# Kernel tuning notes

Hardware: AMD Instinct MI355X
Metric: run time of the kernel (lower is better)

Reference implementation:

```python
import jax, jax.numpy as jnp
import numpy as np

B, H, S, D = 2, 16, 2048, 64

def setup_inputs() -> dict:
    key = jax.random.key(0)
    kq, kk, kv, km = jax.random.split(key, 4)
    Query = jax.random.normal(kq, (B, H, S, D), dtype=jnp.float32)
    Key = jax.random.normal(kk, (B, H, S, D), dtype=jnp.float32)
    Value = jax.random.normal(kv, (B, H, S, D), dtype=jnp.float32)
    attention_mask = jax.random.randint(km, (B, 1, S, S), 0, 2).astype(jnp.bool_)
    return {"Query": Query, "Key": Key, "Value": Value,
            "attention_mask": attention_mask, "dim_key": D}

def reference(Query, Key, Value, attention_mask, dim_key):
    # scores: [B,H,S,S]
    scale = 1.0 / np.sqrt(dim_key).astype(np.float32)
    scores = jnp.einsum('bhqd,bhkd->bhqk', Query, Key) * scale
    scores = jnp.where(attention_mask, jnp.float32(-1e9), scores)
    attention = jax.nn.softmax(scores, axis=-1)
    context = jnp.einsum('bhqk,bhkd->bhqd', attention, Value)
    return (context, attention)
```

## Files before the change

kernel.cpp:

```cpp
#include <hip/hip_runtime.h>
#include <hip/hip_bf16.h>


#define S_LEN 2048
#define D_DIM 64
#define LOG2E 1.44269504088896340736f

typedef __attribute__((ext_vector_type(8))) short bf16x8;
typedef __attribute__((ext_vector_type(4))) float f32x4;
typedef unsigned long long u64;

#define FENCE() asm volatile("" ::: "memory")

__device__ __forceinline__ unsigned int f2bs2(float x, float y) {
    union { __hip_bfloat162 h; unsigned int u; } u;
    u.h = __float22bfloat162_rn(make_float2(x, y));
    return u.u;
}
__device__ __forceinline__ short f2bs(float f) {
    union { __hip_bfloat16 h; short s; } u;
    u.h = __float2bfloat16(f);
    return u.s;
}
__device__ __forceinline__ bf16x8 cvt8(float4 a, float4 b) {
    union { bf16x8 v; unsigned int w[4]; } u;
    u.w[0] = f2bs2(a.x, a.y); u.w[1] = f2bs2(a.z, a.w);
    u.w[2] = f2bs2(b.x, b.y); u.w[3] = f2bs2(b.z, b.w);
    return u.v;
}

__device__ __forceinline__ void gl2lds16(const short* g, short* l) {
    __builtin_amdgcn_global_load_lds(
        (const __attribute__((address_space(1))) unsigned int*)g,
        (__attribute__((address_space(3))) unsigned int*)l, 16, 0, 0);
}

__global__ __launch_bounds__(256) void prep_kv(const float* __restrict__ K,
                                               const float* __restrict__ V,
                                               short* __restrict__ Kb,
                                               short* __restrict__ Vtb) {
    __shared__ short T[64 * 80];
    const int bh = blockIdx.x >> 5;
    const int kt = blockIdx.x & 31;
    const int k0 = kt * 64;
    const int t  = threadIdx.x;
    const int row = t >> 2;
    const int cq  = (t & 3) * 16;

    const size_t base = (size_t)bh * S_LEN * D_DIM;
    {
        const float* kp = K + base + (size_t)(k0 + row) * D_DIM + cq;
        float4 a = ((const float4*)kp)[0], b = ((const float4*)kp)[1],
               c = ((const float4*)kp)[2], d = ((const float4*)kp)[3];
        short* op = Kb + base + (size_t)(k0 + row) * D_DIM + cq;
        *(bf16x8*)op       = cvt8(a, b);
        *(bf16x8*)(op + 8) = cvt8(c, d);
    }
    {
        const float* vp = V + base + (size_t)(k0 + row) * D_DIM + cq;
        float4 a = ((const float4*)vp)[0], b = ((const float4*)vp)[1],
               c = ((const float4*)vp)[2], d = ((const float4*)vp)[3];
        float vv[16] = {a.x,a.y,a.z,a.w, b.x,b.y,b.z,b.w,
                        c.x,c.y,c.z,c.w, d.x,d.y,d.z,d.w};
        #pragma unroll
        for (int i = 0; i < 16; ++i)
            T[(cq + i) * 80 + row] = f2bs(vv[i]);
    }
    __syncthreads();
    {
        const int d  = t >> 2;
        const int kc = (t & 3) * 16;
        short* op = Vtb + (size_t)bh * D_DIM * S_LEN + (size_t)d * S_LEN + k0 + kc;
        *(bf16x8*)op       = *(const bf16x8*)&T[d * 80 + kc];
        *(bf16x8*)(op + 8) = *(const bf16x8*)&T[d * 80 + kc + 8];
    }
}

__global__ __launch_bounds__(256) void mask_pack(const int* __restrict__ M,
                                                 u64* __restrict__ Mp) {
    const int lane = threadIdx.x & 63;
    const int wid  = (blockIdx.x * 256 + threadIdx.x) >> 6;
    const int nwaves = gridDim.x * 4;
    const int nwords = 2 * S_LEN * (S_LEN / 64);
    for (int w = wid; w < nwords; w += nwaves) {
        int v = M[(size_t)w * 64 + lane];
        u64 bits = __ballot(v != 0);
        if (lane == 0) Mp[w] = bits;
    }
}

__global__ __launch_bounds__(256, 4) void sdpa_main(
    const float* __restrict__ Q, const short* __restrict__ Kb,
    const short* __restrict__ Vtb, const u64* __restrict__ Mp,
    float* __restrict__ Ctx, float* __restrict__ Attn)
{
    __shared__ short Kt[2][64 * 64];
    __shared__ short Pt[4 * 16 * 80];

    const int tid  = threadIdx.x;
    const int wave = tid >> 6;
    const int lane = tid & 63;
    const int quad = lane >> 4;
    const int l16  = lane & 15;

    const int bid = blockIdx.x;
    const int bh  = ((bid >> 8) << 3) | (bid & 7);
    const int qt  = (bid >> 3) & 31;
    const int b   = bh >> 4;
    const int qw  = qt * 64 + wave * 16;

    const size_t sd_off = (size_t)bh * S_LEN * D_DIM;
    const float* Qbh = Q + sd_off;
    const short* Kbh = Kb + sd_off;
    const short* Vbh = Vtb + (size_t)bh * D_DIM * S_LEN;
    float* Cbh = Ctx + sd_off;
    float* Abh = Attn + (size_t)bh * S_LEN * S_LEN;

    const short* vfp = Vbh + (size_t)l16 * S_LEN + quad * 8;

    bf16x8 qfrag[2];
    {
        const int qrow = qw + l16;
        const float s = 0.125f * LOG2E;
        #pragma unroll
        for (int kc = 0; kc < 2; ++kc) {
            const float* qp = Qbh + (size_t)qrow * D_DIM + kc * 32 + quad * 8;
            float4 a = ((const float4*)qp)[0], c = ((const float4*)qp)[1];
            a.x*=s; a.y*=s; a.z*=s; a.w*=s; c.x*=s; c.y*=s; c.z*=s; c.w*=s;
            qfrag[kc] = cvt8(a, c);
        }
    }

    const u64* mp = Mp + (size_t)(b * S_LEN + qw + quad * 4) * (S_LEN / 64);

    u64 mw[4], mwn[4];
    float lacc[4] = {0.f, 0.f, 0.f, 0.f};

    #pragma unroll
    for (int r = 0; r < 4; ++r) mw[r] = mp[r * 32];
    #pragma unroll
    for (int rd = 0; rd < 2; ++rd) {
        const int m = tid + rd * 256;
        const int row = m >> 3, sc = m & 7, c = sc ^ (row & 7);
        gl2lds16(Kbh + (size_t)row * D_DIM + c * 8, &Kt[0][m * 8]);
    }
    FENCE();

#define S1_STEP(KT) do {                                                        \
    const int kt_ = (KT);                                                       \
    const int tn_ = (kt_ + 1) & 31; const int p_ = kt_ & 1;                     \
    _Pragma("unroll") for (int r = 0; r < 4; ++r) mwn[r] = mp[r * 32 + tn_];    \
    FENCE();                                                                    \
    asm volatile("s_waitcnt vmcnt(4)" ::: "memory");                            \
    __builtin_amdgcn_s_barrier();                                               \
    __builtin_amdgcn_sched_barrier(0);                                          \
    _Pragma("unroll") for (int rd = 0; rd < 2; ++rd) {                          \
        const int m_ = tid + rd * 256;                                          \
        const int row_ = m_ >> 3, sc_ = m_ & 7, c_ = sc_ ^ (row_ & 7);          \
        gl2lds16(Kbh + (size_t)(tn_ * 64 + row_) * D_DIM + c_ * 8,              \
                 &Kt[p_ ^ 1][m_ * 8]);                                          \
    }                                                                           \
    FENCE();                                                                    \
    __builtin_amdgcn_s_setprio(1);                                              \
    _Pragma("unroll") for (int cc = 0; cc < 4; ++cc) {                          \
        const int keyl_ = cc * 16 + l16;                                        \
        f32x4 acc_ = {0.f, 0.f, 0.f, 0.f};                                      \
        bf16x8 b0_ = *(const bf16x8*)&Kt[p_][keyl_ * 64 + ((quad) ^ (keyl_ & 7)) * 8];      \
        bf16x8 b1_ = *(const bf16x8*)&Kt[p_][keyl_ * 64 + ((4 + quad) ^ (keyl_ & 7)) * 8];  \
        acc_ = __builtin_amdgcn_mfma_f32_16x16x32_bf16(qfrag[0], b0_, acc_, 0, 0, 0);       \
        acc_ = __builtin_amdgcn_mfma_f32_16x16x32_bf16(qfrag[1], b1_, acc_, 0, 0, 0);       \
        _Pragma("unroll") for (int r = 0; r < 4; ++r) {                         \
            float pe_ = __builtin_amdgcn_exp2f(acc_[r]);                        \
            pe_ = ((mw[r] >> keyl_) & 1ull) ? 0.f : pe_;                        \
            lacc[r] += pe_;                                                     \
        }                                                                       \
    }                                                                           \
    __builtin_amdgcn_s_setprio(0);                                              \
    _Pragma("unroll") for (int r = 0; r < 4; ++r) mw[r] = mwn[r];               \
} while (0)

    #pragma unroll 1
    for (int kt = 0; kt < 32; ++kt) S1_STEP(kt);

    #pragma unroll
    for (int off = 1; off < 16; off <<= 1) {
        #pragma unroll
        for (int r = 0; r < 4; ++r) lacc[r] += __shfl_xor(lacc[r], off, 64);
    }
    float inv_l[4];
    #pragma unroll
    for (int r = 0; r < 4; ++r) inv_l[r] = 1.0f / lacc[r];

    f32x4 cacc[4];
    #pragma unroll
    for (int dc = 0; dc < 4; ++dc) cacc[dc] = (f32x4){0.f, 0.f, 0.f, 0.f};
    short* Pw = &Pt[wave * 16 * 80];

#define S2_STEP(KT, WSTR) do {                                                  \
    const int kt_ = (KT); const int k0_ = kt_ * 64;                             \
    const int tn_ = (kt_ + 1) & 31; const int p_ = kt_ & 1;                     \
    _Pragma("unroll") for (int r = 0; r < 4; ++r) mwn[r] = mp[r * 32 + tn_];    \
    bf16x8 vfr[2][4];                                                           \
    _Pragma("unroll") for (int kc = 0; kc < 2; ++kc)                            \
        _Pragma("unroll") for (int dc = 0; dc < 4; ++dc)                        \
            vfr[kc][dc] = *(const bf16x8*)(vfp + (size_t)dc * 16 * S_LEN + k0_ + kc * 32);  \
    FENCE();                                                                    \
    asm volatile("s_waitcnt vmcnt(" WSTR ")" ::: "memory");                     \
    __builtin_amdgcn_s_barrier();                                               \
    __builtin_amdgcn_sched_barrier(0);                                          \
    _Pragma("unroll") for (int rd = 0; rd < 2; ++rd) {                          \
        const int m_ = tid + rd * 256;                                          \
        const int row_ = m_ >> 3, sc_ = m_ & 7, c_ = sc_ ^ (row_ & 7);          \
        gl2lds16(Kbh + (size_t)(tn_ * 64 + row_) * D_DIM + c_ * 8,              \
                 &Kt[p_ ^ 1][m_ * 8]);                                          \
    }                                                                           \
    FENCE();                                                                    \
    __builtin_amdgcn_s_setprio(1);                                              \
    float* ap0_ = Abh + (size_t)(qw + quad * 4) * S_LEN + k0_;                  \
    _Pragma("unroll") for (int cc = 0; cc < 4; ++cc) {                          \
        const int keyl_ = cc * 16 + l16;                                        \
        f32x4 acc_ = {0.f, 0.f, 0.f, 0.f};                                      \
        bf16x8 b0_ = *(const bf16x8*)&Kt[p_][keyl_ * 64 + ((quad) ^ (keyl_ & 7)) * 8];      \
        bf16x8 b1_ = *(const bf16x8*)&Kt[p_][keyl_ * 64 + ((4 + quad) ^ (keyl_ & 7)) * 8];  \
        acc_ = __builtin_amdgcn_mfma_f32_16x16x32_bf16(qfrag[0], b0_, acc_, 0, 0, 0);       \
        acc_ = __builtin_amdgcn_mfma_f32_16x16x32_bf16(qfrag[1], b1_, acc_, 0, 0, 0);       \
        _Pragma("unroll") for (int r = 0; r < 4; ++r) {                         \
            float pe_ = __builtin_amdgcn_exp2f(acc_[r]);                        \
            pe_ = ((mw[r] >> keyl_) & 1ull) ? 0.f : pe_;                        \
            __builtin_nontemporal_store(pe_ * inv_l[r], ap0_ + (size_t)r * S_LEN + keyl_);  \
            Pw[(quad * 4 + r) * 80 + keyl_] = f2bs(pe_);    \
        }                                                                       \
    }                                                                           \
    __builtin_amdgcn_s_setprio(0);                                              \
    FENCE();                                                                    \
    _Pragma("unroll") for (int kc = 0; kc < 2; ++kc) {                          \
        bf16x8 af_ = *(const bf16x8*)&Pw[l16 * 80 + kc * 32 + quad * 8];        \
        _Pragma("unroll") for (int dc = 0; dc < 4; ++dc)                        \
            cacc[dc] = __builtin_amdgcn_mfma_f32_16x16x32_bf16(af_, vfr[kc][dc], cacc[dc], 0, 0, 0); \
    }                                                                           \
    _Pragma("unroll") for (int r = 0; r < 4; ++r) mw[r] = mwn[r];               \
} while (0)

    S2_STEP(0, "12");
    #pragma unroll 1
    for (int kt = 1; kt < 32; ++kt) S2_STEP(kt, "28");

    #pragma unroll
    for (int dc = 0; dc < 4; ++dc) {
        #pragma unroll
        for (int r = 0; r < 4; ++r) {
            Cbh[(size_t)(qw + quad * 4 + r) * D_DIM + dc * 16 + l16] =
                cacc[dc][r] * inv_l[r];
        }
    }
}

extern "C" void kernel_launch(void* const* d_in, const int* in_sizes, int n_in,
                              void* d_out, int out_size, void* d_ws, size_t ws_size,
                              hipStream_t stream) {
    const float* Q    = (const float*)d_in[0];
    const float* K    = (const float*)d_in[1];
    const float* V    = (const float*)d_in[2];
    const int*   Mask = (const int*)d_in[3];

    float* Ctx  = (float*)d_out;
    float* Attn = (float*)d_out + (size_t)2 * 16 * 2048 * 64;

    short* Kb  = (short*)d_ws;
    short* Vtb = (short*)((char*)d_ws + 8388608);
    u64*   Mp  = (u64*)((char*)d_ws + 16777216);

    prep_kv<<<dim3(1024), dim3(256), 0, stream>>>(K, V, Kb, Vtb);
    mask_pack<<<dim3(512), dim3(256), 0, stream>>>(Mask, Mp);
    sdpa_main<<<dim3(1024), dim3(256), 0, stream>>>(Q, Kb, Vtb, Mp, Ctx, Attn);
}
```

Baseline: 752.0 us.

## Transpose QK^T MFMA so each lane owns one query row with vectorized attention stores

Swaps the MFMA operand order so the score tile is transposed, and each lane now holds four consecutive keys of a single query row. Each lane therefore needs one mask word instead of four, the row-sum reduction drops to two shuffles, and attention probabilities go out as 16-byte nontemporal vector stores instead of scalar stores. P is normalized before the bf16 conversion, so the final context scaling is removed. The waitcnt counts are adjusted to match the fewer outstanding loads. The risk is that normalizing before bf16 rounding changes precision slightly, and the hand-tuned waitcnt values must stay exact.

```diff
diff --git a/kernel.cpp b/kernel.cpp
--- a/kernel.cpp
+++ b/kernel.cpp
@@ -131,13 +131,12 @@
         }
     }
 
-    const u64* mp = Mp + (size_t)(b * S_LEN + qw + quad * 4) * (S_LEN / 64);
-
-    u64 mw[4], mwn[4];
-    float lacc[4] = {0.f, 0.f, 0.f, 0.f};
-
-    #pragma unroll
-    for (int r = 0; r < 4; ++r) mw[r] = mp[r * 32];
+    const u64* mp1 = Mp + (size_t)(b * S_LEN + qw + l16) * (S_LEN / 64);
+
+    u64 mw, mwn;
+    float lacc = 0.f;
+
+    mw = mp1[0];
     #pragma unroll
     for (int rd = 0; rd < 2; ++rd) {
         const int m = tid + rd * 256;
@@ -149,9 +148,9 @@
 #define S1_STEP(KT) do {                                                        \
     const int kt_ = (KT);                                                       \
     const int tn_ = (kt_ + 1) & 31; const int p_ = kt_ & 1;                     \
-    _Pragma("unroll") for (int r = 0; r < 4; ++r) mwn[r] = mp[r * 32 + tn_];    \
-    FENCE();                                                                    \
-    asm volatile("s_waitcnt vmcnt(4)" ::: "memory");                            \
+    mwn = mp1[tn_];                                                             \
+    FENCE();                                                                    \
+    asm volatile("s_waitcnt vmcnt(1)" ::: "memory");                            \
     __builtin_amdgcn_s_barrier();                                               \
     __builtin_amdgcn_sched_barrier(0);                                          \
     _Pragma("unroll") for (int rd = 0; rd < 2; ++rd) {                          \
@@ -165,31 +164,27 @@
     _Pragma("unroll") for (int cc = 0; cc < 4; ++cc) {                          \
         const int keyl_ = cc * 16 + l16;                                        \
         f32x4 acc_ = {0.f, 0.f, 0.f, 0.f};                                      \
-        bf16x8 b0_ = *(const bf16x8*)&Kt[p_][keyl_ * 64 + ((quad) ^ (keyl_ & 7)) * 8];      \
-        bf16x8 b1_ = *(const bf16x8*)&Kt[p_][keyl_ * 64 + ((4 + quad) ^ (keyl_ & 7)) * 8];  \
-        acc_ = __builtin_amdgcn_mfma_f32_16x16x32_bf16(qfrag[0], b0_, acc_, 0, 0, 0);       \
-        acc_ = __builtin_amdgcn_mfma_f32_16x16x32_bf16(qfrag[1], b1_, acc_, 0, 0, 0);       \
+        bf16x8 k0f_ = *(const bf16x8*)&Kt[p_][keyl_ * 64 + ((quad) ^ (keyl_ & 7)) * 8];     \
+        bf16x8 k1f_ = *(const bf16x8*)&Kt[p_][keyl_ * 64 + ((4 + quad) ^ (keyl_ & 7)) * 8]; \
+        acc_ = __builtin_amdgcn_mfma_f32_16x16x32_bf16(k0f_, qfrag[0], acc_, 0, 0, 0);      \
+        acc_ = __builtin_amdgcn_mfma_f32_16x16x32_bf16(k1f_, qfrag[1], acc_, 0, 0, 0);      \
+        const unsigned bits_ = (unsigned)(mw >> (cc * 16 + quad * 4));          \
         _Pragma("unroll") for (int r = 0; r < 4; ++r) {                         \
             float pe_ = __builtin_amdgcn_exp2f(acc_[r]);                        \
-            pe_ = ((mw[r] >> keyl_) & 1ull) ? 0.f : pe_;                        \
-            lacc[r] += pe_;                                                     \
+            pe_ = ((bits_ >> r) & 1u) ? 0.f : pe_;                              \
+            lacc += pe_;                                                        \
         }                                                                       \
     }                                                                           \
     __builtin_amdgcn_s_setprio(0);                                              \
-    _Pragma("unroll") for (int r = 0; r < 4; ++r) mw[r] = mwn[r];               \
+    mw = mwn;                                                                   \
 } while (0)
 
     #pragma unroll 1
     for (int kt = 0; kt < 32; ++kt) S1_STEP(kt);
 
-    #pragma unroll
-    for (int off = 1; off < 16; off <<= 1) {
-        #pragma unroll
-        for (int r = 0; r < 4; ++r) lacc[r] += __shfl_xor(lacc[r], off, 64);
-    }
-    float inv_l[4];
-    #pragma unroll
-    for (int r = 0; r < 4; ++r) inv_l[r] = 1.0f / lacc[r];
+    lacc += __shfl_xor(lacc, 16, 64);
+    lacc += __shfl_xor(lacc, 32, 64);
+    const float inv_l = 1.0f / lacc;
 
     f32x4 cacc[4];
     #pragma unroll
@@ -199,7 +194,7 @@
 #define S2_STEP(KT, WSTR) do {                                                  \
     const int kt_ = (KT); const int k0_ = kt_ * 64;                             \
     const int tn_ = (kt_ + 1) & 31; const int p_ = kt_ & 1;                     \
-    _Pragma("unroll") for (int r = 0; r < 4; ++r) mwn[r] = mp[r * 32 + tn_];    \
+    mwn = mp1[tn_];                                                             \
     bf16x8 vfr[2][4];                                                           \
     _Pragma("unroll") for (int kc = 0; kc < 2; ++kc)                            \
         _Pragma("unroll") for (int dc = 0; dc < 4; ++dc)                        \
@@ -216,20 +211,26 @@
     }                                                                           \
     FENCE();                                                                    \
     __builtin_amdgcn_s_setprio(1);                                              \
-    float* ap0_ = Abh + (size_t)(qw + quad * 4) * S_LEN + k0_;                  \
+    float* ap_ = Abh + (size_t)(qw + l16) * S_LEN + k0_ + quad * 4;             \
     _Pragma("unroll") for (int cc = 0; cc < 4; ++cc) {                          \
         const int keyl_ = cc * 16 + l16;                                        \
         f32x4 acc_ = {0.f, 0.f, 0.f, 0.f};                                      \
-        bf16x8 b0_ = *(const bf16x8*)&Kt[p_][keyl_ * 64 + ((quad) ^ (keyl_ & 7)) * 8];      \
-        bf16x8 b1_ = *(const bf16x8*)&Kt[p_][keyl_ * 64 + ((4 + quad) ^ (keyl_ & 7)) * 8];  \
-        acc_ = __builtin_amdgcn_mfma_f32_16x16x32_bf16(qfrag[0], b0_, acc_, 0, 0, 0);       \
-        acc_ = __builtin_amdgcn_mfma_f32_16x16x32_bf16(qfrag[1], b1_, acc_, 0, 0, 0);       \
+        bf16x8 k0f_ = *(const bf16x8*)&Kt[p_][keyl_ * 64 + ((quad) ^ (keyl_ & 7)) * 8];     \
+        bf16x8 k1f_ = *(const bf16x8*)&Kt[p_][keyl_ * 64 + ((4 + quad) ^ (keyl_ & 7)) * 8]; \
+        acc_ = __builtin_amdgcn_mfma_f32_16x16x32_bf16(k0f_, qfrag[0], acc_, 0, 0, 0);      \
+        acc_ = __builtin_amdgcn_mfma_f32_16x16x32_bf16(k1f_, qfrag[1], acc_, 0, 0, 0);      \
+        const unsigned bits_ = (unsigned)(mw >> (cc * 16 + quad * 4));          \
+        f32x4 pn_;                                                              \
         _Pragma("unroll") for (int r = 0; r < 4; ++r) {                         \
             float pe_ = __builtin_amdgcn_exp2f(acc_[r]);                        \
-            pe_ = ((mw[r] >> keyl_) & 1ull) ? 0.f : pe_;                        \
-            __builtin_nontemporal_store(pe_ * inv_l[r], ap0_ + (size_t)r * S_LEN + keyl_);  \
-            Pw[(quad * 4 + r) * 80 + keyl_] = f2bs(pe_);    \
+            pe_ = ((bits_ >> r) & 1u) ? 0.f : pe_;                              \
+            pn_[r] = pe_ * inv_l;                               \
         }                                                                       \
+        __builtin_nontemporal_store(pn_, (f32x4*)(ap_ + cc * 16));              \
+          \
+        union { unsigned w[2]; u64 d; } pk_;                                    \
+        pk_.w[0] = f2bs2(pn_[0], pn_[1]); pk_.w[1] = f2bs2(pn_[2], pn_[3]);     \
+        *(u64*)&Pw[l16 * 80 + cc * 16 + quad * 4] = pk_.d;                      \
     }                                                                           \
     __builtin_amdgcn_s_setprio(0);                                              \
     FENCE();                                                                    \
@@ -238,19 +239,18 @@
         _Pragma("unroll") for (int dc = 0; dc < 4; ++dc)                        \
             cacc[dc] = __builtin_amdgcn_mfma_f32_16x16x32_bf16(af_, vfr[kc][dc], cacc[dc], 0, 0, 0); \
     }                                                                           \
-    _Pragma("unroll") for (int r = 0; r < 4; ++r) mw[r] = mwn[r];               \
+    mw = mwn;                                                                   \
 } while (0)
 
-    S2_STEP(0, "12");
+    S2_STEP(0, "9");
     #pragma unroll 1
-    for (int kt = 1; kt < 32; ++kt) S2_STEP(kt, "28");
+    for (int kt = 1; kt < 32; ++kt) S2_STEP(kt, "13");
 
     #pragma unroll
     for (int dc = 0; dc < 4; ++dc) {
         #pragma unroll
         for (int r = 0; r < 4; ++r) {
-            Cbh[(size_t)(qw + quad * 4 + r) * D_DIM + dc * 16 + l16] =
-                cacc[dc][r] * inv_l[r];
+            Cbh[(size_t)(qw + quad * 4 + r) * D_DIM + dc * 16 + l16] = cacc[dc][r];
         }
     }
 }
```

After: 747.8 us. About the same (-0.6%).
